# Performance work log

Hardware: AMD Instinct MI355X
Metric: run time of the kernel (lower is better)

## Reference

```python
import jax, jax.numpy as jnp
import numpy as np

G_MIN = 0.01

def _st(x):
    # straight-through: fwd zeroes |x|<G_MIN, bwd is identity
    hard = jnp.where(jnp.abs(x) < G_MIN, 0.0, x)
    return x + jax.lax.stop_gradient(hard - x)

def _inv(x):
    return 0.104 - 0.899 * jnp.tanh((x + 0.056) * 3.858)

def _activate(z):
    return 0.134 + 0.962 * jnp.tanh((z - 0.183) * 24.1)

def setup_inputs() -> dict:
    key = jax.random.key(0)
    k1, k2, k3 = jax.random.split(key, 3)
    M, n_in, n_out = 8192, 4096, 4096
    a_previous = jax.random.uniform(k1, (M, n_in), dtype=jnp.float32)
    theta = jax.random.uniform(k2, (n_out, n_in + 2), dtype=jnp.float32)
    # mimic __init__ scaling of last two columns
    theta = theta.at[:, -1].multiply(100.0)
    theta = theta.at[:, -2].set(0.1788 / (1 - 0.1788) * (jnp.sum(jnp.abs(theta[:, :-3]), axis=1) + jnp.abs(theta[:, -1])))
    aging_decay = jax.random.uniform(k3, (n_out, n_in + 2), minval=0.9, maxval=1.0, dtype=jnp.float32)
    return {"a_previous": a_previous, "theta": theta, "aging_decay": aging_decay}

def reference(a_previous, theta, aging_decay):
    M = a_previous.shape[0]
    # aged + straight-through theta
    th = _st(theta * aging_decay)                     # [m, n]
    g = jnp.abs(th)
    W = g / jnp.sum(g, axis=1, keepdims=True)         # [m, n]
    # augment input with ones and zeros columns
    a_aug = jnp.concatenate([a_previous,
                             jnp.ones((M, 1), a_previous.dtype),
                             jnp.zeros((M, 1), a_previous.dtype)], axis=1)  # [M, n]
    inv_a = _inv(a_aug)
    pt = (th >= 0).astype(W.dtype)
    nt = (th < 0).astype(W.dtype)
    # z[j,i] = sum_k a_aug[j,k]*W[i,k]*pt[i,k] + inv_a[j,k]*W[i,k]*nt[i,k]
    z = a_aug @ (W * pt).T + inv_a @ (W * nt).T       # [M, m]
    return _activate(z)
```

## Files before the change

### kernel.cpp

```cpp
#include <hip/hip_runtime.h>
#include <hip/hip_bf16.h>
#include <stdint.h>

#define M_DIM 8192
#define N_DIM 4096
#define K_IN  4096
#define NC    (K_IN + 2)
#define K_DIM (2 * K_IN)

#define BM 256
#define BN 256
#define BKB 128
#define NT (K_DIM / BKB)

typedef __attribute__((ext_vector_type(4))) int i32x4;
typedef __attribute__((ext_vector_type(16))) int i32x16;

__device__ __forceinline__ float fast_tanh(float y) {
  float e = __expf(2.0f * y);
  return 1.0f - 2.0f * __builtin_amdgcn_rcpf(1.0f + e);
}

__device__ __forceinline__ int q8(float x) {
  return (int)__builtin_rintf(x);
}

__global__ __launch_bounds__(256) void prep_A(const float* __restrict__ a,
                                              int8_t* __restrict__ Ap) {
  int idx = blockIdx.x * 256 + threadIdx.x;
  int j  = idx >> 10;
  int k4 = (idx & 1023) << 2;
  float4 v = reinterpret_cast<const float4*>(a)[idx];
  float xs[4] = {v.x, v.y, v.z, v.w};
  int lw = 0, rw = 0;
#pragma unroll
  for (int t = 0; t < 4; ++t) {
    float x = xs[t];
    int ql = q8(x * 127.0f);
    float inv = 0.104f - 0.899f * fast_tanh((x + 0.056f) * 3.858f);
    int qr = q8(inv * 127.0f);
    lw |= (ql & 255) << (8 * t);
    rw |= (qr & 255) << (8 * t);
  }
  size_t base = (size_t)j * K_DIM + k4;
  *reinterpret_cast<int*>(Ap + base)        = lw;
  *reinterpret_cast<int*>(Ap + base + K_IN) = rw;
}

__global__ __launch_bounds__(256) void prep_B(const float* __restrict__ theta,
                                              const float* __restrict__ aging,
                                              int8_t* __restrict__ Bp,
                                              float* __restrict__ corr,
                                              float* __restrict__ sc) {
  __shared__ float th_s[NC];
  __shared__ float red_s[256];
  __shared__ float red_m[256];
  int i = blockIdx.x;
  int tid = threadIdx.x;
  const float* tr = theta + (size_t)i * NC;
  const float* ar = aging + (size_t)i * NC;
  float psum = 0.f, pmax = 0.f;
  for (int k = tid; k < NC; k += 256) {
    float th = tr[k] * ar[k];
    if (fabsf(th) < 0.01f) th = 0.f;
    th_s[k] = th;
    psum += fabsf(th);
    if (k < K_IN) pmax = fmaxf(pmax, fabsf(th));
  }
  red_s[tid] = psum;
  red_m[tid] = pmax;
  __syncthreads();
  for (int s = 128; s > 0; s >>= 1) {
    if (tid < s) {
      red_s[tid] += red_s[tid + s];
      red_m[tid] = fmaxf(red_m[tid], red_m[tid + s]);
    }
    __syncthreads();
  }
  float inv_sum = 1.0f / red_s[0];
  float maxabs  = red_m[0];
  float qs = 127.0f / maxabs;
  int8_t* out = Bp + (size_t)i * K_DIM;
  for (int k0 = tid * 4; k0 < K_IN; k0 += 1024) {
    int pw = 0, nw = 0;
#pragma unroll
    for (int t = 0; t < 4; ++t) {
      float th = th_s[k0 + t];
      int q = q8(fabsf(th) * qs);
      if (th >= 0.f) pw |= (q & 255) << (8 * t);
      else           nw |= (q & 255) << (8 * t);
    }
    *reinterpret_cast<int*>(out + k0)         = pw;
    *reinterpret_cast<int*>(out + K_IN + k0)  = nw;
  }
  if (tid == 0) {
    float th1 = th_s[K_IN];
    float th2 = th_s[K_IN + 1];
    float w1 = fabsf(th1) * inv_sum;
    float w2 = fabsf(th2) * inv_sum;
    float inv1 = 0.104f - 0.899f * fast_tanh((1.0f + 0.056f) * 3.858f);
    float inv0 = 0.104f - 0.899f * fast_tanh((0.0f + 0.056f) * 3.858f);
    float c = (th1 >= 0.f) ? w1 : w1 * inv1;
    c += (th2 >= 0.f) ? 0.0f : w2 * inv0;
    corr[i] = c;
    sc[i] = maxabs * inv_sum * (1.0f / 16129.0f);
  }
}

__global__ __launch_bounds__(512, 2) void gemm_fused(const int8_t* __restrict__ A,
                                                     const int8_t* __restrict__ B,
                                                     const float* __restrict__ corr,
                                                     const float* __restrict__ sc,
                                                     float* __restrict__ C) {
  extern __shared__ char lds[];
  const int tid  = threadIdx.x;
  const int lane = tid & 63;
  const int wid  = tid >> 6;
  const int wr   = wid >> 2;
  const int wc   = wid & 3;
  const int fr   = lane & 31;
  const int kg   = lane >> 5;

  const int bid = (int)blockIdx.x;
  const int sw  = (bid & 7) * 64 + (bid >> 3);
  const int bm0 = (sw >> 4) * BM;
  const int bn0 = (sw & 15) * BN;

  const int colsw = (((tid & 7) ^ ((tid >> 3) & 7) ^ ((tid >> 6) & 3)) << 4);
  const int8_t* gA = A + (size_t)(bm0 + (tid >> 3)) * K_DIM + colsw;
  const int8_t* gB = B + (size_t)(bn0 + (tid >> 3)) * K_DIM + colsw;
  const int dst_t = tid * 16;

  const int flip = (((fr & 7) ^ ((fr >> 3) & 3)) << 4);
  int csk[4];
#pragma unroll
  for (int ks = 0; ks < 4; ++ks) csk[ks] = (ks * 32 + kg * 16) ^ flip;
  const int aRow = (wr * 128 + fr) * BKB;
  const int bRow = (wc * 64 + fr) * BKB;

  i32x16 acc[4][2] = {};

#define STAGE(ISA, H, T) do {                                                        \
    const int8_t* _g = (ISA) ? gA : gB;                                              \
    const size_t _go = (size_t)((H) * 128) * K_DIM + (size_t)(T) * BKB;              \
    char* _l = lds + (((T) & 1) * 65536) + ((ISA) ? 0 : 32768) + (H) * 16384 + dst_t; \
    __builtin_amdgcn_global_load_lds(                                                \
        (const __attribute__((address_space(1))) unsigned int*)(_g + _go),           \
        (__attribute__((address_space(3))) unsigned int*)_l, 16, 0, 0);              \
    __builtin_amdgcn_global_load_lds(                                                \
        (const __attribute__((address_space(1))) unsigned int*)(_g + _go + (size_t)64 * K_DIM), \
        (__attribute__((address_space(3))) unsigned int*)(_l + 8192), 16, 0, 0);     \
  } while (0)

#define MFMA32(a, b, c) __builtin_amdgcn_mfma_i32_32x32x32_i8((a), (b), (c), 0, 0, 0)

  STAGE(0, 0, 0); STAGE(0, 1, 0); STAGE(1, 0, 0); STAGE(1, 1, 0);
  STAGE(0, 0, 1); STAGE(0, 1, 1); STAGE(1, 0, 1); STAGE(1, 1, 1);
  asm volatile("s_waitcnt vmcnt(8)" ::: "memory");
  __builtin_amdgcn_s_barrier();

#pragma unroll 2
  for (int W = 0; W < NT; ++W) {
    const char* pa = lds + (W & 1) * 65536 + aRow;
    const char* pb = lds + (W & 1) * 65536 + 32768 + bRow;
    i32x4 af[2][4], bf[2][4];

#pragma unroll
    for (int m = 0; m < 2; ++m)
#pragma unroll
      for (int ks = 0; ks < 4; ++ks)
        af[m][ks] = *(const i32x4*)(pa + m * 32 * BKB + csk[ks]);
#pragma unroll
    for (int ks = 0; ks < 4; ++ks)
      bf[0][ks] = *(const i32x4*)(pb + csk[ks]);
    __builtin_amdgcn_s_barrier();
    asm volatile("s_waitcnt lgkmcnt(0)" ::: "memory");
    __builtin_amdgcn_sched_barrier(0);
    __builtin_amdgcn_s_setprio(1);
#pragma unroll
    for (int m = 0; m < 2; ++m)
#pragma unroll
      for (int ks = 0; ks < 4; ++ks)
        acc[m][0] = MFMA32(af[m][ks], bf[0][ks], acc[m][0]);
    __builtin_amdgcn_s_setprio(0);

#pragma unroll
    for (int ks = 0; ks < 4; ++ks)
      bf[1][ks] = *(const i32x4*)(pb + 32 * BKB + csk[ks]);
    __builtin_amdgcn_s_barrier();
    asm volatile("s_waitcnt lgkmcnt(0)" ::: "memory");
    __builtin_amdgcn_sched_barrier(0);
    __builtin_amdgcn_s_setprio(1);
#pragma unroll
    for (int m = 0; m < 2; ++m)
#pragma unroll
      for (int ks = 0; ks < 4; ++ks)
        acc[m][1] = MFMA32(af[m][ks], bf[1][ks], acc[m][1]);
    __builtin_amdgcn_s_setprio(0);

#pragma unroll
    for (int m = 0; m < 2; ++m)
#pragma unroll
      for (int ks = 0; ks < 4; ++ks)
        af[m][ks] = *(const i32x4*)(pa + (m + 2) * 32 * BKB + csk[ks]);
    if (W + 2 < NT) { STAGE(0, 0, W + 2); STAGE(0, 1, W + 2); }
    __builtin_amdgcn_s_barrier();
    asm volatile("s_waitcnt lgkmcnt(0)" ::: "memory");
    __builtin_amdgcn_sched_barrier(0);
    __builtin_amdgcn_s_setprio(1);
#pragma unroll
    for (int m = 0; m < 2; ++m)
#pragma unroll
      for (int ks = 0; ks < 4; ++ks)
        acc[m + 2][0] = MFMA32(af[m][ks], bf[0][ks], acc[m + 2][0]);
    __builtin_amdgcn_s_setprio(0);

    if (W + 2 < NT) { STAGE(1, 0, W + 2); STAGE(1, 1, W + 2); }
    if (W < NT - 2) { asm volatile("s_waitcnt vmcnt(8)" ::: "memory"); }
    else            { asm volatile("s_waitcnt vmcnt(0)" ::: "memory"); }
    __builtin_amdgcn_s_barrier();
    __builtin_amdgcn_sched_barrier(0);
    __builtin_amdgcn_s_setprio(1);
#pragma unroll
    for (int m = 0; m < 2; ++m)
#pragma unroll
      for (int ks = 0; ks < 4; ++ks)
        acc[m + 2][1] = MFMA32(af[m][ks], bf[1][ks], acc[m + 2][1]);
    __builtin_amdgcn_s_setprio(0);
  }

#pragma unroll
  for (int n = 0; n < 2; ++n) {
    const int col = bn0 + wc * 64 + n * 32 + fr;
    const float cr = corr[col];
    const float s  = sc[col];
#pragma unroll
    for (int mi = 0; mi < 4; ++mi) {
      const int rbase = bm0 + wr * 128 + mi * 32 + 4 * kg;
#pragma unroll
      for (int r = 0; r < 16; ++r) {
        const int row = rbase + (r & 3) + 8 * (r >> 2);
        float z = (float)acc[mi][n][r] * s + cr;
        float e = __expf((z - 0.183f) * 48.2f);
        C[(size_t)row * N_DIM + col] = 1.096f - 1.924f * __builtin_amdgcn_rcpf(1.0f + e);
      }
    }
  }
#undef STAGE
#undef MFMA32
}

extern "C" void kernel_launch(void* const* d_in, const int* in_sizes, int n_in,
                              void* d_out, int out_size, void* d_ws, size_t ws_size,
                              hipStream_t stream) {
  (void)in_sizes; (void)n_in; (void)out_size; (void)ws_size;
  const float* a_prev = (const float*)d_in[0];
  const float* theta  = (const float*)d_in[1];
  const float* aging  = (const float*)d_in[2];
  float* out = (float*)d_out;

  char* ws = (char*)d_ws;
  int8_t* Ap = (int8_t*)ws;
  int8_t* Bp = (int8_t*)(ws + (size_t)M_DIM * K_DIM);
  float* corr = (float*)(ws + (size_t)M_DIM * K_DIM + (size_t)N_DIM * K_DIM);
  float* sc   = corr + N_DIM;

  prep_A<<<(M_DIM * K_IN / 4) / 256, 256, 0, stream>>>(a_prev, Ap);
  prep_B<<<N_DIM, 256, 0, stream>>>(theta, aging, Bp, corr, sc);

  (void)hipFuncSetAttribute((const void*)gemm_fused,
                            hipFuncAttributeMaxDynamicSharedMemorySize, 131072);
  gemm_fused<<<dim3((M_DIM / BM) * (N_DIM / BN)), dim3(512), 131072, stream>>>(Ap, Bp, corr, sc, out);
}
```

Baseline: 298.0 us.

## Collapse four-phase GEMM main loop into two phases with B prefetched one tile ahead

Reworks the int8 MFMA main loop from four barrier-separated compute phases into two. Each phase now loads both B fragments up front and issues 16 MFMAs interleaved over ks, m and n. B tiles are now staged one iteration ahead instead of two, with the prologue and vmcnt thresholds adjusted to match. This halves the barriers and LDS-wait stalls per K tile and gives longer MFMA runs, at the cost of more live B fragment registers and a shorter prefetch distance for B.

```diff
diff --git a/kernel.cpp b/kernel.cpp
--- a/kernel.cpp
+++ b/kernel.cpp
@@ -154,9 +154,9 @@
 
 #define MFMA32(a, b, c) __builtin_amdgcn_mfma_i32_32x32x32_i8((a), (b), (c), 0, 0, 0)
 
-  STAGE(0, 0, 0); STAGE(0, 1, 0); STAGE(1, 0, 0); STAGE(1, 1, 0);
-  STAGE(0, 0, 1); STAGE(0, 1, 1); STAGE(1, 0, 1); STAGE(1, 1, 1);
-  asm volatile("s_waitcnt vmcnt(8)" ::: "memory");
+  STAGE(1, 0, 0); STAGE(1, 1, 0); STAGE(0, 0, 0); STAGE(0, 1, 0);
+  STAGE(0, 0, 1); STAGE(0, 1, 1);
+  asm volatile("s_waitcnt vmcnt(4)" ::: "memory");
   __builtin_amdgcn_s_barrier();
 
 #pragma unroll 2
@@ -171,61 +171,43 @@
       for (int ks = 0; ks < 4; ++ks)
         af[m][ks] = *(const i32x4*)(pa + m * 32 * BKB + csk[ks]);
 #pragma unroll
-    for (int ks = 0; ks < 4; ++ks)
-      bf[0][ks] = *(const i32x4*)(pb + csk[ks]);
+    for (int n = 0; n < 2; ++n)
+#pragma unroll
+      for (int ks = 0; ks < 4; ++ks)
+        bf[n][ks] = *(const i32x4*)(pb + n * 32 * BKB + csk[ks]);
+    if (W + 1 < NT) { STAGE(1, 0, W + 1); STAGE(1, 1, W + 1); }
     __builtin_amdgcn_s_barrier();
     asm volatile("s_waitcnt lgkmcnt(0)" ::: "memory");
     __builtin_amdgcn_sched_barrier(0);
     __builtin_amdgcn_s_setprio(1);
 #pragma unroll
+    for (int ks = 0; ks < 4; ++ks)
+#pragma unroll
+      for (int m = 0; m < 2; ++m)
+#pragma unroll
+        for (int n = 0; n < 2; ++n)
+          acc[m][n] = MFMA32(af[m][ks], bf[n][ks], acc[m][n]);
+    __builtin_amdgcn_s_setprio(0);
+
+#pragma unroll
     for (int m = 0; m < 2; ++m)
 #pragma unroll
       for (int ks = 0; ks < 4; ++ks)
-        acc[m][0] = MFMA32(af[m][ks], bf[0][ks], acc[m][0]);
-    __builtin_amdgcn_s_setprio(0);
-
-#pragma unroll
-    for (int ks = 0; ks < 4; ++ks)
-      bf[1][ks] = *(const i32x4*)(pb + 32 * BKB + csk[ks]);
+        af[m][ks] = *(const i32x4*)(pa + (m + 2) * 32 * BKB + csk[ks]);
+    if (W + 2 < NT) { STAGE(0, 0, W + 2); STAGE(0, 1, W + 2); }
+    if (W < NT - 2) { asm volatile("s_waitcnt vmcnt(4)" ::: "memory"); }
+    else            { asm volatile("s_waitcnt vmcnt(0)" ::: "memory"); }
     __builtin_amdgcn_s_barrier();
     asm volatile("s_waitcnt lgkmcnt(0)" ::: "memory");
     __builtin_amdgcn_sched_barrier(0);
     __builtin_amdgcn_s_setprio(1);
 #pragma unroll
-    for (int m = 0; m < 2; ++m)
-#pragma unroll
-      for (int ks = 0; ks < 4; ++ks)
-        acc[m][1] = MFMA32(af[m][ks], bf[1][ks], acc[m][1]);
-    __builtin_amdgcn_s_setprio(0);
-
-#pragma unroll
-    for (int m = 0; m < 2; ++m)
-#pragma unroll
-      for (int ks = 0; ks < 4; ++ks)
-        af[m][ks] = *(const i32x4*)(pa + (m + 2) * 32 * BKB + csk[ks]);
-    if (W + 2 < NT) { STAGE(0, 0, W + 2); STAGE(0, 1, W + 2); }
-    __builtin_amdgcn_s_barrier();
-    asm volatile("s_waitcnt lgkmcnt(0)" ::: "memory");
-    __builtin_amdgcn_sched_barrier(0);
-    __builtin_amdgcn_s_setprio(1);
-#pragma unroll
-    for (int m = 0; m < 2; ++m)
-#pragma unroll
-      for (int ks = 0; ks < 4; ++ks)
-        acc[m + 2][0] = MFMA32(af[m][ks], bf[0][ks], acc[m + 2][0]);
-    __builtin_amdgcn_s_setprio(0);
-
-    if (W + 2 < NT) { STAGE(1, 0, W + 2); STAGE(1, 1, W + 2); }
-    if (W < NT - 2) { asm volatile("s_waitcnt vmcnt(8)" ::: "memory"); }
-    else            { asm volatile("s_waitcnt vmcnt(0)" ::: "memory"); }
-    __builtin_amdgcn_s_barrier();
-    __builtin_amdgcn_sched_barrier(0);
-    __builtin_amdgcn_s_setprio(1);
-#pragma unroll
-    for (int m = 0; m < 2; ++m)
-#pragma unroll
-      for (int ks = 0; ks < 4; ++ks)
-        acc[m + 2][1] = MFMA32(af[m][ks], bf[1][ks], acc[m + 2][1]);
+    for (int ks = 0; ks < 4; ++ks)
+#pragma unroll
+      for (int m = 0; m < 2; ++m)
+#pragma unroll
+        for (int n = 0; n < 2; ++n)
+          acc[m + 2][n] = MFMA32(af[m][ks], bf[n][ks], acc[m + 2][n]);
     __builtin_amdgcn_s_setprio(0);
   }
 
```

Result: no change. 303.6 us (+1.9%).
